# Optimization experiments

Hardware: AMD Instinct MI355X
Metric: run time of the kernel (lower is better)

Reference implementation:

```python
import jax, jax.numpy as jnp
import numpy as np

B, D, L = 64, 1024, 2048  # batch, init dim, source length; context feature dim = D//2


def setup_inputs() -> dict:
    key = jax.random.key(0)
    k1, k2, k3, k4 = jax.random.split(key, 4)
    inp = jax.random.normal(k1, (B, D), dtype=jnp.float32)
    context = jax.random.normal(k2, (B, L, D // 2), dtype=jnp.float32)
    # torch Linear weights: [out_features, in_features]
    W_in = jax.random.normal(k3, (D, D), dtype=jnp.float32) * (1.0 / np.sqrt(D))
    W_out = jax.random.normal(k4, (D, 2 * D), dtype=jnp.float32) * (1.0 / np.sqrt(2 * D))
    return {"input": inp, "context": context, "W_in": W_in, "W_out": W_out}


def reference(input, context, W_in, W_out):
    Bv, Dv = input.shape
    # linear_in(input).view(B, D//2, 2): two query vectors of size D//2 per batch
    targetT = (input @ W_in.T).reshape(Bv, Dv // 2, 2)           # [B, D/2, 2]
    attn = jnp.einsum('bld,bdk->bkl', context, targetT)          # [B, 2, L]
    attn = jax.nn.softmax(attn, axis=-1)                         # softmax over sourceL
    weighted = jnp.einsum('bkl,bld->bkd', attn, context)         # [B, 2, D/2]
    weightedContext = weighted.reshape(Bv, Dv)                   # [B, D]
    combined = jnp.concatenate([weightedContext, input], axis=1) # [B, 2D]
    contextOutput = jnp.tanh(combined @ W_out.T)                 # [B, D]
    return contextOutput, attn[:, 0, :], attn[:, 1, :]
```

## Files before the change

kernel.cpp:

```cpp
#include <hip/hip_runtime.h>
#include <cmath>

#define NB 64
#define ND 1024
#define DH 512
#define NL 2048
#define NCHUNK 16
#define RPB 128
#define RPW 32
#define REC 520
#define KS 8

template <int KK>
__global__ __launch_bounds__(256) void k_gemm(const float* __restrict__ A,
                                              const float* __restrict__ W,
                                              float* __restrict__ part) {
  constexpr int SLAB = KK / KS;
  __shared__ float As[64][36];
  const int t = threadIdx.x;
  const int lane = t & 63;
  const int wv = t >> 6;
  const int k0 = blockIdx.y * SLAB;
  const int j0 = __builtin_amdgcn_readfirstlane((int)(blockIdx.x * 32 + wv * 8));
  const float* Wb = W + (size_t)j0 * KK + k0;

  float acc[8];
#pragma unroll
  for (int j = 0; j < 8; j++) acc[j] = 0.f;

  const int srow = t >> 2, sko = (t & 3) * 8;
  const float* sbase = A + (size_t)srow * KK + k0 + sko;

  for (int kc = 0; kc < SLAB; kc += 32) {
    float4 v0 = *(const float4*)(sbase + kc);
    float4 v1 = *(const float4*)(sbase + kc + 4);
    __syncthreads();
    *(float4*)&As[srow][sko]     = v0;
    *(float4*)&As[srow][sko + 4] = v1;
    __syncthreads();
#pragma unroll
    for (int kk = 0; kk < 32; kk += 4) {
      float4 av = *(const float4*)&As[lane][kk];
      const float* wp = Wb + kc + kk;
#pragma unroll
      for (int j = 0; j < 8; j++) {
        float4 wq = *(const float4*)(wp + (size_t)j * KK);
        acc[j] = fmaf(av.x, wq.x, acc[j]);
        acc[j] = fmaf(av.y, wq.y, acc[j]);
        acc[j] = fmaf(av.z, wq.z, acc[j]);
        acc[j] = fmaf(av.w, wq.w, acc[j]);
      }
    }
  }
  float* p = part + ((size_t)blockIdx.y * 64 + lane) * ND + j0;
#pragma unroll
  for (int j = 0; j < 8; j++) p[j] = acc[j];
}

template <int ACT>
__global__ __launch_bounds__(256) void k_reduce(const float* __restrict__ part,
                                                float* __restrict__ out) {
  const int i = (blockIdx.x * 256 + threadIdx.x) * 4;
  float4 s = make_float4(0.f, 0.f, 0.f, 0.f);
#pragma unroll
  for (int ks = 0; ks < KS; ks++) {
    float4 v = *(const float4*)(part + (size_t)ks * (64 * ND) + i);
    s.x += v.x; s.y += v.y; s.z += v.z; s.w += v.w;
  }
  if (ACT) { s.x = tanhf(s.x); s.y = tanhf(s.y); s.z = tanhf(s.z); s.w = tanhf(s.w); }
  *(float4*)(out + i) = s;
}

__global__ __launch_bounds__(256, 4) void k2_attn(const float* __restrict__ ctx,
                                                  const float* __restrict__ tgt,
                                                  float* __restrict__ sc0,
                                                  float* __restrict__ sc1,
                                                  float* __restrict__ part) {
  const int chunk = blockIdx.x, b = blockIdx.y;
  const int wave = threadIdx.x >> 6, lane = threadIdx.x & 63;
  const float* crow = ctx + ((size_t)b * NL + chunk * RPB + wave * RPW) * DH + lane * 8;

  float t0[8], t1[8];
  {
    const float* tp = tgt + b * ND + lane * 16;
#pragma unroll
    for (int j = 0; j < 4; j++) {
      float4 v = *(const float4*)(tp + j * 4);
      t0[2 * j] = v.x; t1[2 * j] = v.y; t0[2 * j + 1] = v.z; t1[2 * j + 1] = v.w;
    }
  }

  float m0 = -INFINITY, l0 = 0.f, m1 = -INFINITY, l1 = 0.f;
  float a0[8], a1[8];
#pragma unroll
  for (int j = 0; j < 8; j++) { a0[j] = 0.f; a1[j] = 0.f; }
  float sv0 = 0.f, sv1 = 0.f;

  float4 cur[4], nxt[4];
  cur[0] = *(const float4*)(crow);
  cur[1] = *(const float4*)(crow + 4);
  cur[2] = *(const float4*)(crow + DH);
  cur[3] = *(const float4*)(crow + DH + 4);

#pragma unroll 2
  for (int ib = 0; ib < 16; ib++) {
    if (ib < 15) {
      const float* p = crow + (size_t)(2 * ib + 2) * DH;
      nxt[0] = *(const float4*)(p);
      nxt[1] = *(const float4*)(p + 4);
      nxt[2] = *(const float4*)(p + DH);
      nxt[3] = *(const float4*)(p + DH + 4);
    }
    const float* C = (const float*)cur;

    float s0[2], s1[2];
#pragma unroll
    for (int r = 0; r < 2; r++) {
      float x0 = 0.f, x1 = 0.f;
#pragma unroll
      for (int j = 0; j < 8; j++) { x0 += C[r * 8 + j] * t0[j]; x1 += C[r * 8 + j] * t1[j]; }
      s0[r] = x0; s1[r] = x1;
    }
#pragma unroll
    for (int off = 32; off; off >>= 1) {
      s0[0] += __shfl_xor(s0[0], off);
      s0[1] += __shfl_xor(s0[1], off);
      s1[0] += __shfl_xor(s1[0], off);
      s1[1] += __shfl_xor(s1[1], off);
    }
#pragma unroll
    for (int r = 0; r < 2; r++)
      if (lane == 2 * ib + r) { sv0 = s0[r]; sv1 = s1[r]; }

    {
      float mn = fmaxf(m0, fmaxf(s0[0], s0[1]));
      float al = __expf(m0 - mn);
      float p0 = __expf(s0[0] - mn), p1 = __expf(s0[1] - mn);
      l0 = l0 * al + p0 + p1;
      m0 = mn;
#pragma unroll
      for (int j = 0; j < 8; j++)
        a0[j] = a0[j] * al + p0 * C[j] + p1 * C[8 + j];
    }
    {
      float mn = fmaxf(m1, fmaxf(s1[0], s1[1]));
      float al = __expf(m1 - mn);
      float p0 = __expf(s1[0] - mn), p1 = __expf(s1[1] - mn);
      l1 = l1 * al + p0 + p1;
      m1 = mn;
#pragma unroll
      for (int j = 0; j < 8; j++)
        a1[j] = a1[j] * al + p0 * C[j] + p1 * C[8 + j];
    }
#pragma unroll
    for (int i = 0; i < 4; i++) cur[i] = nxt[i];
  }

  const int rowbase = b * NL + chunk * RPB + wave * RPW;
  if (lane < RPW) { sc0[rowbase + lane] = sv0; sc1[rowbase + lane] = sv1; }

  __shared__ float accS[4][1024];
  __shared__ float mlS[4][4];
#pragma unroll
  for (int j = 0; j < 8; j++) {
    accS[wave][lane * 8 + j] = a0[j];
    accS[wave][512 + lane * 8 + j] = a1[j];
  }
  if (lane == 0) { mlS[wave][0] = m0; mlS[wave][1] = l0; mlS[wave][2] = m1; mlS[wave][3] = l1; }
  __syncthreads();

  const int t = threadIdx.x;
  const int k = (t * 4) >> 9;
  const int d = (t * 4) & 511;
  float M = fmaxf(fmaxf(mlS[0][2 * k], mlS[1][2 * k]), fmaxf(mlS[2][2 * k], mlS[3][2 * k]));
  float Lk = 0.f;
  float v0 = 0.f, v1 = 0.f, v2 = 0.f, v3 = 0.f;
#pragma unroll
  for (int w = 0; w < 4; w++) {
    float e = __expf(mlS[w][2 * k] - M);
    Lk += mlS[w][2 * k + 1] * e;
    const float* ap = &accS[w][k * 512 + d];
    v0 += ap[0] * e; v1 += ap[1] * e; v2 += ap[2] * e; v3 += ap[3] * e;
  }
  float* rec = part + ((size_t)(b * NCHUNK + chunk) * 2 + k) * REC;
  if ((t & 127) == 0) { rec[0] = M; rec[1] = Lk; }
  rec[4 + d] = v0; rec[5 + d] = v1; rec[6 + d] = v2; rec[7 + d] = v3;
}

__global__ __launch_bounds__(256) void k3_combine(const float* __restrict__ part,
                                                  const float* __restrict__ inp,
                                                  float* __restrict__ combined,
                                                  float* __restrict__ sc0,
                                                  float* __restrict__ sc1) {
  const int b = blockIdx.x;
  const int t = threadIdx.x;
  __shared__ float MM[2], LL[2];
  if (t < 2) {
    const int k = t;
    float Mk = -INFINITY;
    for (int c = 0; c < NCHUNK; c++)
      Mk = fmaxf(Mk, part[((size_t)(b * NCHUNK + c) * 2 + k) * REC]);
    float Lk = 0.f;
    for (int c = 0; c < NCHUNK; c++) {
      const float* rec = part + ((size_t)(b * NCHUNK + c) * 2 + k) * REC;
      Lk += rec[1] * __expf(rec[0] - Mk);
    }
    MM[k] = Mk; LL[k] = Lk;
  }
  __syncthreads();

  const int k = (t * 4) >> 9, d = (t * 4) & 511;
  float v0 = 0.f, v1 = 0.f, v2 = 0.f, v3 = 0.f;
  for (int c = 0; c < NCHUNK; c++) {
    const float* rec = part + ((size_t)(b * NCHUNK + c) * 2 + k) * REC;
    float e = __expf(rec[0] - MM[k]);
    v0 += rec[4 + d] * e; v1 += rec[5 + d] * e; v2 += rec[6 + d] * e; v3 += rec[7 + d] * e;
  }
  const float inv = 1.f / LL[k];
  float* cp = combined + (size_t)b * 2048 + k * 512 + d;
  cp[0] = v0 * inv; cp[1] = v1 * inv; cp[2] = v2 * inv; cp[3] = v3 * inv;

  const float4 iv = *(const float4*)(inp + (size_t)b * ND + t * 4);
  *(float4*)(combined + (size_t)b * 2048 + 1024 + t * 4) = iv;

  const float M0 = MM[0], i0 = 1.f / LL[0];
  const float M1 = MM[1], i1 = 1.f / LL[1];
#pragma unroll
  for (int r = 0; r < 8; r++) {
    const int idx = b * NL + t * 8 + r;
    sc0[idx] = __expf(sc0[idx] - M0) * i0;
    sc1[idx] = __expf(sc1[idx] - M1) * i1;
  }
}

extern "C" void kernel_launch(void* const* d_in, const int* in_sizes, int n_in,
                              void* d_out, int out_size, void* d_ws, size_t ws_size,
                              hipStream_t stream) {
  const float* input   = (const float*)d_in[0];
  const float* context = (const float*)d_in[1];
  const float* W_in    = (const float*)d_in[2];
  const float* W_out   = (const float*)d_in[3];

  float* out   = (float*)d_out;
  float* attn0 = out + NB * ND;
  float* attn1 = attn0 + NB * NL;

  float* ws       = (float*)d_ws;
  float* target   = ws;
  float* combined = target + NB * ND;
  float* apart    = combined + NB * 2048;
  float* gpart    = apart + NB * NCHUNK * 2 * REC;

  k_gemm<ND><<<dim3(32, KS), dim3(256), 0, stream>>>(input, W_in, gpart);
  k_reduce<0><<<dim3(64), dim3(256), 0, stream>>>(gpart, target);
  k2_attn<<<dim3(NCHUNK, NB), dim3(256), 0, stream>>>(context, target, attn0, attn1, apart);
  k3_combine<<<dim3(NB), dim3(256), 0, stream>>>(apart, input, combined, attn0, attn1);
  k_gemm<2 * ND><<<dim3(32, KS), dim3(256), 0, stream>>>(combined, W_out, gpart);
  k_reduce<1><<<dim3(64), dim3(256), 0, stream>>>(gpart, out);
}
```

Baseline: 451.5 us.

## Widen split-K, use nontemporal context loads, and split combine across more blocks

```diff
diff --git a/kernel.cpp b/kernel.cpp
--- a/kernel.cpp
+++ b/kernel.cpp
@@ -9,12 +9,17 @@
 #define RPB 128
 #define RPW 32
 #define REC 520
-#define KS 8
+#define KS 32
+
+typedef float f4 __attribute__((ext_vector_type(4)));
+__device__ __forceinline__ f4 ntld(const float* p) {
+  return __builtin_nontemporal_load((const f4*)p);
+}
 
 template <int KK>
-__global__ __launch_bounds__(256) void k_gemm(const float* __restrict__ A,
-                                              const float* __restrict__ W,
-                                              float* __restrict__ part) {
+__global__ __launch_bounds__(256, 4) void k_gemm(const float* __restrict__ A,
+                                                 const float* __restrict__ W,
+                                                 float* __restrict__ part) {
   constexpr int SLAB = KK / KS;
   __shared__ float As[64][36];
   const int t = threadIdx.x;
@@ -53,16 +58,16 @@
     }
   }
   float* p = part + ((size_t)blockIdx.y * 64 + lane) * ND + j0;
-#pragma unroll
-  for (int j = 0; j < 8; j++) p[j] = acc[j];
+  *(float4*)(p)     = make_float4(acc[0], acc[1], acc[2], acc[3]);
+  *(float4*)(p + 4) = make_float4(acc[4], acc[5], acc[6], acc[7]);
 }
 
 template <int ACT>
-__global__ __launch_bounds__(256) void k_reduce(const float* __restrict__ part,
-                                                float* __restrict__ out) {
-  const int i = (blockIdx.x * 256 + threadIdx.x) * 4;
+__global__ __launch_bounds__(64) void k_reduce(const float* __restrict__ part,
+                                               float* __restrict__ out) {
+  const int i = (blockIdx.x * 64 + threadIdx.x) * 4;
   float4 s = make_float4(0.f, 0.f, 0.f, 0.f);
-#pragma unroll
+#pragma unroll 8
   for (int ks = 0; ks < KS; ks++) {
     float4 v = *(const float4*)(part + (size_t)ks * (64 * ND) + i);
     s.x += v.x; s.y += v.y; s.z += v.z; s.w += v.w;
@@ -96,20 +101,20 @@
   for (int j = 0; j < 8; j++) { a0[j] = 0.f; a1[j] = 0.f; }
   float sv0 = 0.f, sv1 = 0.f;
 
-  float4 cur[4], nxt[4];
-  cur[0] = *(const float4*)(crow);
-  cur[1] = *(const float4*)(crow + 4);
-  cur[2] = *(const float4*)(crow + DH);
-  cur[3] = *(const float4*)(crow + DH + 4);
+  f4 cur[4], nxt[4];
+  cur[0] = ntld(crow);
+  cur[1] = ntld(crow + 4);
+  cur[2] = ntld(crow + DH);
+  cur[3] = ntld(crow + DH + 4);
 
 #pragma unroll 2
   for (int ib = 0; ib < 16; ib++) {
     if (ib < 15) {
       const float* p = crow + (size_t)(2 * ib + 2) * DH;
-      nxt[0] = *(const float4*)(p);
-      nxt[1] = *(const float4*)(p + 4);
-      nxt[2] = *(const float4*)(p + DH);
-      nxt[3] = *(const float4*)(p + DH + 4);
+      nxt[0] = ntld(p);
+      nxt[1] = ntld(p + 4);
+      nxt[2] = ntld(p + DH);
+      nxt[3] = ntld(p + DH + 4);
     }
     const float* C = (const float*)cur;
 
@@ -184,7 +189,7 @@
   }
   float* rec = part + ((size_t)(b * NCHUNK + chunk) * 2 + k) * REC;
   if ((t & 127) == 0) { rec[0] = M; rec[1] = Lk; }
-  rec[4 + d] = v0; rec[5 + d] = v1; rec[6 + d] = v2; rec[7 + d] = v3;
+  *(float4*)&rec[4 + d] = make_float4(v0, v1, v2, v3);
 }
 
 __global__ __launch_bounds__(256) void k3_combine(const float* __restrict__ part,
@@ -192,15 +197,18 @@
                                                   float* __restrict__ combined,
                                                   float* __restrict__ sc0,
                                                   float* __restrict__ sc1) {
-  const int b = blockIdx.x;
+  const int b = blockIdx.x >> 2, q = blockIdx.x & 3;
   const int t = threadIdx.x;
   __shared__ float MM[2], LL[2];
+  __shared__ float eS[2][NCHUNK];
   if (t < 2) {
     const int k = t;
     float Mk = -INFINITY;
+#pragma unroll
     for (int c = 0; c < NCHUNK; c++)
       Mk = fmaxf(Mk, part[((size_t)(b * NCHUNK + c) * 2 + k) * REC]);
     float Lk = 0.f;
+#pragma unroll
     for (int c = 0; c < NCHUNK; c++) {
       const float* rec = part + ((size_t)(b * NCHUNK + c) * 2 + k) * REC;
       Lk += rec[1] * __expf(rec[0] - Mk);
@@ -208,29 +216,30 @@
     MM[k] = Mk; LL[k] = Lk;
   }
   __syncthreads();
-
-  const int k = (t * 4) >> 9, d = (t * 4) & 511;
-  float v0 = 0.f, v1 = 0.f, v2 = 0.f, v3 = 0.f;
-  for (int c = 0; c < NCHUNK; c++) {
-    const float* rec = part + ((size_t)(b * NCHUNK + c) * 2 + k) * REC;
-    float e = __expf(rec[0] - MM[k]);
-    v0 += rec[4 + d] * e; v1 += rec[5 + d] * e; v2 += rec[6 + d] * e; v3 += rec[7 + d] * e;
-  }
-  const float inv = 1.f / LL[k];
-  float* cp = combined + (size_t)b * 2048 + k * 512 + d;
-  cp[0] = v0 * inv; cp[1] = v1 * inv; cp[2] = v2 * inv; cp[3] = v3 * inv;
-
-  const float4 iv = *(const float4*)(inp + (size_t)b * ND + t * 4);
-  *(float4*)(combined + (size_t)b * 2048 + 1024 + t * 4) = iv;
+  if (t < 2 * NCHUNK) {
+    const int k = t >> 4, c = t & 15;
+    eS[k][c] = __expf(part[((size_t)(b * NCHUNK + c) * 2 + k) * REC] - MM[k]);
+  }
+  __syncthreads();
+
+  const int k = t >> 7, d = q * 128 + (t & 127);
+  float v = 0.f;
+#pragma unroll
+  for (int c = 0; c < NCHUNK; c++)
+    v += part[((size_t)(b * NCHUNK + c) * 2 + k) * REC + 4 + d] * eS[k][c];
+  combined[(size_t)b * 2048 + k * 512 + d] = v / LL[k];
+
+  combined[(size_t)b * 2048 + 1024 + q * 256 + t] = inp[(size_t)b * ND + q * 256 + t];
 
   const float M0 = MM[0], i0 = 1.f / LL[0];
   const float M1 = MM[1], i1 = 1.f / LL[1];
-#pragma unroll
-  for (int r = 0; r < 8; r++) {
-    const int idx = b * NL + t * 8 + r;
-    sc0[idx] = __expf(sc0[idx] - M0) * i0;
-    sc1[idx] = __expf(sc1[idx] - M1) * i1;
-  }
+  const int pos = b * NL + q * 512 + t * 2;
+  float2 x0 = *(const float2*)(sc0 + pos);
+  float2 x1 = *(const float2*)(sc1 + pos);
+  x0.x = __expf(x0.x - M0) * i0; x0.y = __expf(x0.y - M0) * i0;
+  x1.x = __expf(x1.x - M1) * i1; x1.y = __expf(x1.y - M1) * i1;
+  *(float2*)(sc0 + pos) = x0;
+  *(float2*)(sc1 + pos) = x1;
 }
 
 extern "C" void kernel_launch(void* const* d_in, const int* in_sizes, int n_in,
@@ -252,9 +261,9 @@
   float* gpart    = apart + NB * NCHUNK * 2 * REC;
 
   k_gemm<ND><<<dim3(32, KS), dim3(256), 0, stream>>>(input, W_in, gpart);
-  k_reduce<0><<<dim3(64), dim3(256), 0, stream>>>(gpart, target);
+  k_reduce<0><<<dim3(256), dim3(64), 0, stream>>>(gpart, target);
   k2_attn<<<dim3(NCHUNK, NB), dim3(256), 0, stream>>>(context, target, attn0, attn1, apart);
-  k3_combine<<<dim3(NB), dim3(256), 0, stream>>>(apart, input, combined, attn0, attn1);
+  k3_combine<<<dim3(4 * NB), dim3(256), 0, stream>>>(apart, input, combined, attn0, attn1);
   k_gemm<2 * ND><<<dim3(32, KS), dim3(256), 0, stream>>>(combined, W_out, gpart);
-  k_reduce<1><<<dim3(64), dim3(256), 0, stream>>>(gpart, out);
-}
+  k_reduce<1><<<dim3(256), dim3(64), 0, stream>>>(gpart, out);
+}
```

Result: faster. 391.5 us (-13.3%).
